# Performance work log

Measured on AMD Instinct MI355X. Metric: run time of the kernel, lower is better.

The kernel has to match this reference:

```python
import jax, jax.numpy as jnp
from jax import lax
import numpy as np

N, W, H, C = 32, 64, 64, 256
D_STYLE = 256


def setup_inputs() -> dict:
    key = jax.random.key(0)
    k1, k2, k3, k4 = jax.random.split(key, 4)
    inputs = jax.random.normal(k1, (N, W, H, C), dtype=jnp.float32)
    style_coding = jax.random.normal(k2, (N, D_STYLE), dtype=jnp.float32)
    # he_normal-ish init scaling for the learned weights
    w_dense = jax.random.normal(k3, (D_STYLE, C), dtype=jnp.float32) * np.sqrt(2.0 / D_STYLE)
    w_conv = jax.random.normal(k4, (1, 1, C, C), dtype=jnp.float32) * np.sqrt(2.0 / C)
    return {"inputs": inputs, "style_coding": style_coding, "w_dense": w_dense, "w_conv": w_conv}


def reference(inputs, style_coding, w_dense, w_conv):
    # inputs: [N,W,H,C] (NHWC), style_coding: [N,D_style]
    c = inputs.shape[-1]
    scale = 1.0 / jnp.sqrt(jnp.float32(c))
    # Dense(fout_dim, use_bias=False, activation=LeakyReLU())  (keras default alpha=0.3)
    q = jax.nn.leaky_relu(style_coding @ w_dense, negative_slope=0.3)  # [N,C]
    # channel-wise attention: einsum('nwhc,nwhc->nc') with q broadcast over w,h
    ca_logits = jnp.einsum('nwhc,nc->nc', inputs, q) * scale           # [N,C]
    ca = jax.nn.softmax(ca_logits, axis=-1)[:, None, None, :]          # [N,1,1,C]
    # position-wise attention: einsum('nwhc,nwhc->nwh'), softmax over flattened W*H
    pa_logits = jnp.einsum('nwhc,nc->nwh', inputs, q) * scale          # [N,W,H]
    n, w, h = pa_logits.shape
    pa = jax.nn.softmax(pa_logits.reshape(n, w * h), axis=1).reshape(n, w, h, 1)
    x = inputs * ca * pa                                               # [N,W,H,C]
    # DarknetConv2D_BN_Leaky with no norm kwarg: 1x1 conv (no bias) + LeakyReLU(0.1)
    y = lax.conv_general_dilated(x, w_conv, window_strides=(1, 1), padding='SAME',
                                 dimension_numbers=('NHWC', 'HWIO', 'NHWC'))
    return jax.nn.leaky_relu(y, negative_slope=0.1)
```

## Files before the change

### kernel.cpp

```cpp
#include <hip/hip_runtime.h>
#include <hip/hip_bf16.h>


#define NBATCH 32
#define PIX 4096
#define CH 256
#define SCALE 0.0625f

typedef __attribute__((ext_vector_type(8))) short short8;
typedef __attribute__((ext_vector_type(4))) short short4v;
typedef __attribute__((ext_vector_type(4))) float floatx4;

__device__ __forceinline__ short f2bf(float x) {
    unsigned u = __builtin_bit_cast(unsigned, x);
    u += 0x7fffu + ((u >> 16) & 1u);
    return (short)(u >> 16);
}

__global__ __launch_bounds__(256) void style_kernel(
    const float* __restrict__ style, const float* __restrict__ wd,
    float* __restrict__ q, float* __restrict__ colsum)
{
    __shared__ float s[256];
    const int n = blockIdx.x, t = threadIdx.x;
    s[t] = style[n * 256 + t];
    __syncthreads();
    float acc = 0.f;
#pragma unroll 8
    for (int k = 0; k < 256; ++k) acc += s[k] * wd[k * 256 + t];
    q[n * 256 + t] = acc > 0.f ? acc : 0.3f * acc;
    colsum[n * 256 + t] = 0.f;
}

__global__ void wt_kernel(const float* __restrict__ wc, short* __restrict__ wT)
{
    __shared__ float tile[32][33];
    const int co0 = blockIdx.x * 32, ci0 = blockIdx.y * 32;
    const int tx = threadIdx.x, ty = threadIdx.y;
#pragma unroll
    for (int r = 0; r < 4; ++r)
        tile[ty + r * 8][tx] = wc[(ci0 + ty + r * 8) * 256 + co0 + tx];
    __syncthreads();
#pragma unroll
    for (int r = 0; r < 4; ++r)
        wT[(co0 + ty + r * 8) * 256 + ci0 + tx] = f2bf(tile[tx][ty + r * 8]);
}

__global__ __launch_bounds__(256) void reduce_kernel(
    const float* __restrict__ inp, const float* __restrict__ q,
    float* __restrict__ colsum, float* __restrict__ pa_logits)
{
    const int n = blockIdx.y;
    const int chunk = blockIdx.x;
    const int lane = threadIdx.x & 63, w = threadIdx.x >> 6;
    const float4 qv = *(const float4*)&q[n * 256 + lane * 4];
    float4 cs = make_float4(0.f, 0.f, 0.f, 0.f);
    const int pbase = chunk * 128 + w * 32;
    const float* base = inp + ((size_t)n * PIX + pbase) * CH;
    for (int j = 0; j < 32; ++j) {
        float4 v = *(const float4*)&base[(size_t)j * CH + lane * 4];
        float d = v.x * qv.x + v.y * qv.y + v.z * qv.z + v.w * qv.w;
        cs.x += v.x; cs.y += v.y; cs.z += v.z; cs.w += v.w;
#pragma unroll
        for (int off = 32; off; off >>= 1) d += __shfl_xor(d, off);
        if (lane == 0) pa_logits[n * PIX + pbase + j] = d * SCALE;
    }
    float* cp = colsum + n * 256 + lane * 4;
    atomicAdd(cp + 0, cs.x);
    atomicAdd(cp + 1, cs.y);
    atomicAdd(cp + 2, cs.z);
    atomicAdd(cp + 3, cs.w);
}

__global__ __launch_bounds__(256) void softmax_kernel(
    const float* __restrict__ colsum, const float* __restrict__ q,
    const float* __restrict__ pa_logits,
    float* __restrict__ ca, float* __restrict__ pa)
{
    __shared__ float red[256];
    const int n = blockIdx.x, t = threadIdx.x;

    float lg = colsum[n * 256 + t] * q[n * 256 + t] * SCALE;
    red[t] = lg; __syncthreads();
    for (int s = 128; s > 0; s >>= 1) {
        if (t < s) red[t] = fmaxf(red[t], red[t + s]);
        __syncthreads();
    }
    float m = red[0]; __syncthreads();
    float e = expf(lg - m);
    red[t] = e; __syncthreads();
    for (int s = 128; s > 0; s >>= 1) {
        if (t < s) red[t] += red[t + s];
        __syncthreads();
    }
    ca[n * 256 + t] = e / red[0];
    __syncthreads();

    float lv[16];
    float lmax = -1e30f;
#pragma unroll
    for (int i = 0; i < 16; ++i) {
        lv[i] = pa_logits[n * PIX + t + 256 * i];
        lmax = fmaxf(lmax, lv[i]);
    }
    red[t] = lmax; __syncthreads();
    for (int s = 128; s > 0; s >>= 1) {
        if (t < s) red[t] = fmaxf(red[t], red[t + s]);
        __syncthreads();
    }
    float M = red[0]; __syncthreads();
    float ev[16], lsum = 0.f;
#pragma unroll
    for (int i = 0; i < 16; ++i) { ev[i] = expf(lv[i] - M); lsum += ev[i]; }
    red[t] = lsum; __syncthreads();
    for (int s = 128; s > 0; s >>= 1) {
        if (t < s) red[t] += red[t + s];
        __syncthreads();
    }
    float inv = 1.0f / red[0];
#pragma unroll
    for (int i = 0; i < 16; ++i) pa[n * PIX + t + 256 * i] = ev[i] * inv;
}

__global__ __launch_bounds__(256) void conv_mfma(
    const float* __restrict__ inp, const float* __restrict__ ca,
    const float* __restrict__ pa, const short* __restrict__ wT,
    float* __restrict__ out)
{
    __shared__ __attribute__((aligned(16))) short As[128][72];
    __shared__ __attribute__((aligned(16))) short Bs[128][72];

    const int n   = blockIdx.z;
    const int m0  = blockIdx.y * 128;
    const int co0 = blockIdx.x * 128;
    const int tid = threadIdx.x;
    const int lane = tid & 63, wid = tid >> 6;
    const int wm = wid & 1, wn = wid >> 1;
    const int l16 = lane & 15, quad = lane >> 4;

    floatx4 acc[4][4] = {};

    const float* Abase = inp + ((size_t)(n * PIX + m0)) * CH;
    const short* Bbase = wT + (size_t)co0 * CH;

    const int akq = tid & 15, arb = tid >> 4;
    const int bck = tid & 7,  brb = tid >> 3;

    for (int kb = 0; kb < 4; ++kb) {
        const int k0 = kb * 64;
        if (kb) __syncthreads();
        const float4 cav = *(const float4*)&ca[n * 256 + k0 + akq * 4];
#pragma unroll
        for (int i = 0; i < 8; ++i) {
            const int r = arb + 16 * i;
            float4 v = *(const float4*)&Abase[(size_t)r * CH + k0 + akq * 4];
            short4v s;
            s.x = f2bf(v.x * cav.x);
            s.y = f2bf(v.y * cav.y);
            s.z = f2bf(v.z * cav.z);
            s.w = f2bf(v.w * cav.w);
            *(short4v*)&As[r][akq * 4] = s;
        }
#pragma unroll
        for (int i = 0; i < 4; ++i) {
            const int r = brb + 32 * i;
            *(uint4*)&Bs[r][bck * 8] = *(const uint4*)&Bbase[(size_t)r * CH + k0 + bck * 8];
        }
        __syncthreads();
#pragma unroll
        for (int kk = 0; kk < 64; kk += 32) {
            short8 af[4], bfr[4];
#pragma unroll
            for (int mt = 0; mt < 4; ++mt)
                af[mt] = *(const short8*)&As[wm * 64 + mt * 16 + l16][kk + quad * 8];
#pragma unroll
            for (int nt = 0; nt < 4; ++nt)
                bfr[nt] = *(const short8*)&Bs[wn * 64 + nt * 16 + l16][kk + quad * 8];
#pragma unroll
            for (int mt = 0; mt < 4; ++mt)
#pragma unroll
                for (int nt = 0; nt < 4; ++nt)
                    acc[mt][nt] = __builtin_amdgcn_mfma_f32_16x16x32_bf16(
                        af[mt], bfr[nt], acc[mt][nt], 0, 0, 0);
        }
    }

#pragma unroll
    for (int mt = 0; mt < 4; ++mt) {
#pragma unroll
        for (int reg = 0; reg < 4; ++reg) {
            const int pix = m0 + wm * 64 + mt * 16 + quad * 4 + reg;
            const float pav = pa[n * PIX + pix];
            float* orow = out + ((size_t)(n * PIX + pix)) * CH + co0 + wn * 64;
#pragma unroll
            for (int nt = 0; nt < 4; ++nt) {
                float z = acc[mt][nt][reg] * pav;
                orow[nt * 16 + l16] = z > 0.f ? z : 0.1f * z;
            }
        }
    }
}

extern "C" void kernel_launch(void* const* d_in, const int* in_sizes, int n_in,
                              void* d_out, int out_size, void* d_ws, size_t ws_size,
                              hipStream_t stream) {
    const float* inputs = (const float*)d_in[0];
    const float* style  = (const float*)d_in[1];
    const float* wdense = (const float*)d_in[2];
    const float* wconv  = (const float*)d_in[3];
    float* out = (float*)d_out;

    char* ws = (char*)d_ws;
    float* q         = (float*)(ws + 0);
    float* colsum    = (float*)(ws + 32768);
    float* ca        = (float*)(ws + 65536);
    float* pa_logits = (float*)(ws + 98304);
    float* pa        = (float*)(ws + 622592);
    short* wT        = (short*)(ws + 1146880);

    style_kernel<<<NBATCH, 256, 0, stream>>>(style, wdense, q, colsum);
    wt_kernel<<<dim3(8, 8), dim3(32, 8), 0, stream>>>(wconv, wT);
    reduce_kernel<<<dim3(32, NBATCH), 256, 0, stream>>>(inputs, q, colsum, pa_logits);
    softmax_kernel<<<NBATCH, 256, 0, stream>>>(colsum, q, pa_logits, ca, pa);
    conv_mfma<<<dim3(2, 32, NBATCH), 256, 0, stream>>>(inputs, ca, pa, wT, out);
}
```

Measured before the change: 313.9 us.

## Fold channel attention into per-batch weights and pre-convert inputs to bf16

```diff
diff --git a/kernel.cpp b/kernel.cpp
--- a/kernel.cpp
+++ b/kernel.cpp
@@ -32,24 +32,12 @@
     colsum[n * 256 + t] = 0.f;
 }
 
-__global__ void wt_kernel(const float* __restrict__ wc, short* __restrict__ wT)
-{
-    __shared__ float tile[32][33];
-    const int co0 = blockIdx.x * 32, ci0 = blockIdx.y * 32;
-    const int tx = threadIdx.x, ty = threadIdx.y;
-#pragma unroll
-    for (int r = 0; r < 4; ++r)
-        tile[ty + r * 8][tx] = wc[(ci0 + ty + r * 8) * 256 + co0 + tx];
-    __syncthreads();
-#pragma unroll
-    for (int r = 0; r < 4; ++r)
-        wT[(co0 + ty + r * 8) * 256 + ci0 + tx] = f2bf(tile[tx][ty + r * 8]);
-}
-
-__global__ __launch_bounds__(256) void reduce_kernel(
+__global__ __launch_bounds__(256) void reduce_convert_kernel(
     const float* __restrict__ inp, const float* __restrict__ q,
-    float* __restrict__ colsum, float* __restrict__ pa_logits)
-{
+    float* __restrict__ colsum, float* __restrict__ pa_logits,
+    short* __restrict__ in_bf)
+{
+    __shared__ float sm[4][256];
     const int n = blockIdx.y;
     const int chunk = blockIdx.x;
     const int lane = threadIdx.x & 63, w = threadIdx.x >> 6;
@@ -57,19 +45,23 @@
     float4 cs = make_float4(0.f, 0.f, 0.f, 0.f);
     const int pbase = chunk * 128 + w * 32;
     const float* base = inp + ((size_t)n * PIX + pbase) * CH;
+    short* bfb = in_bf + ((size_t)n * PIX + pbase) * CH;
     for (int j = 0; j < 32; ++j) {
         float4 v = *(const float4*)&base[(size_t)j * CH + lane * 4];
+        short4v s;
+        s.x = f2bf(v.x); s.y = f2bf(v.y); s.z = f2bf(v.z); s.w = f2bf(v.w);
+        *(short4v*)&bfb[(size_t)j * CH + lane * 4] = s;
         float d = v.x * qv.x + v.y * qv.y + v.z * qv.z + v.w * qv.w;
         cs.x += v.x; cs.y += v.y; cs.z += v.z; cs.w += v.w;
 #pragma unroll
         for (int off = 32; off; off >>= 1) d += __shfl_xor(d, off);
         if (lane == 0) pa_logits[n * PIX + pbase + j] = d * SCALE;
     }
-    float* cp = colsum + n * 256 + lane * 4;
-    atomicAdd(cp + 0, cs.x);
-    atomicAdd(cp + 1, cs.y);
-    atomicAdd(cp + 2, cs.z);
-    atomicAdd(cp + 3, cs.w);
+    *(float4*)&sm[w][lane * 4] = cs;
+    __syncthreads();
+    const int t = threadIdx.x;
+    float tot = sm[0][t] + sm[1][t] + sm[2][t] + sm[3][t];
+    atomicAdd(&colsum[n * 256 + t], tot);
 }
 
 __global__ __launch_bounds__(256) void softmax_kernel(
@@ -122,10 +114,31 @@
     for (int i = 0; i < 16; ++i) pa[n * PIX + t + 256 * i] = ev[i] * inv;
 }
 
+__global__ void fold_kernel(const float* __restrict__ wc,
+                            const float* __restrict__ ca,
+                            short* __restrict__ wn)
+{
+    __shared__ float tile[32][33];
+    const int co0 = blockIdx.x * 32, n = blockIdx.y;
+    const int tx = threadIdx.x, ty = threadIdx.y;
+    short* wout = wn + (size_t)n * 65536;
+    for (int cit = 0; cit < 8; ++cit) {
+        const int ci0 = cit * 32;
+        if (cit) __syncthreads();
+#pragma unroll
+        for (int r = 0; r < 4; ++r)
+            tile[ty + r * 8][tx] = wc[(ci0 + ty + r * 8) * 256 + co0 + tx];
+        __syncthreads();
+        const float cav = ca[n * 256 + ci0 + tx];
+#pragma unroll
+        for (int r = 0; r < 4; ++r)
+            wout[(co0 + ty + r * 8) * 256 + ci0 + tx] = f2bf(tile[tx][ty + r * 8] * cav);
+    }
+}
+
 __global__ __launch_bounds__(256) void conv_mfma(
-    const float* __restrict__ inp, const float* __restrict__ ca,
-    const float* __restrict__ pa, const short* __restrict__ wT,
-    float* __restrict__ out)
+    const short* __restrict__ in_bf, const float* __restrict__ pa,
+    const short* __restrict__ wn, float* __restrict__ out)
 {
     __shared__ __attribute__((aligned(16))) short As[128][72];
     __shared__ __attribute__((aligned(16))) short Bs[128][72];
@@ -135,36 +148,24 @@
     const int co0 = blockIdx.x * 128;
     const int tid = threadIdx.x;
     const int lane = tid & 63, wid = tid >> 6;
-    const int wm = wid & 1, wn = wid >> 1;
+    const int wm = wid & 1, wn_ = wid >> 1;
     const int l16 = lane & 15, quad = lane >> 4;
 
     floatx4 acc[4][4] = {};
 
-    const float* Abase = inp + ((size_t)(n * PIX + m0)) * CH;
-    const short* Bbase = wT + (size_t)co0 * CH;
-
-    const int akq = tid & 15, arb = tid >> 4;
-    const int bck = tid & 7,  brb = tid >> 3;
+    const short* Abase = in_bf + ((size_t)(n * PIX + m0)) * CH;
+    const short* Bbase = wn + (size_t)n * 65536 + (size_t)co0 * CH;
+
+    const int g = tid & 7, r0 = tid >> 3;
 
     for (int kb = 0; kb < 4; ++kb) {
         const int k0 = kb * 64;
         if (kb) __syncthreads();
-        const float4 cav = *(const float4*)&ca[n * 256 + k0 + akq * 4];
-#pragma unroll
-        for (int i = 0; i < 8; ++i) {
-            const int r = arb + 16 * i;
-            float4 v = *(const float4*)&Abase[(size_t)r * CH + k0 + akq * 4];
-            short4v s;
-            s.x = f2bf(v.x * cav.x);
-            s.y = f2bf(v.y * cav.y);
-            s.z = f2bf(v.z * cav.z);
-            s.w = f2bf(v.w * cav.w);
-            *(short4v*)&As[r][akq * 4] = s;
-        }
 #pragma unroll
         for (int i = 0; i < 4; ++i) {
-            const int r = brb + 32 * i;
-            *(uint4*)&Bs[r][bck * 8] = *(const uint4*)&Bbase[(size_t)r * CH + k0 + bck * 8];
+            const int r = r0 + 32 * i;
+            *(uint4*)&As[r][g * 8] = *(const uint4*)&Abase[(size_t)r * CH + k0 + g * 8];
+            *(uint4*)&Bs[r][g * 8] = *(const uint4*)&Bbase[(size_t)r * CH + k0 + g * 8];
         }
         __syncthreads();
 #pragma unroll
@@ -175,7 +176,7 @@
                 af[mt] = *(const short8*)&As[wm * 64 + mt * 16 + l16][kk + quad * 8];
 #pragma unroll
             for (int nt = 0; nt < 4; ++nt)
-                bfr[nt] = *(const short8*)&Bs[wn * 64 + nt * 16 + l16][kk + quad * 8];
+                bfr[nt] = *(const short8*)&Bs[wn_ * 64 + nt * 16 + l16][kk + quad * 8];
 #pragma unroll
             for (int mt = 0; mt < 4; ++mt)
 #pragma unroll
@@ -191,7 +192,7 @@
         for (int reg = 0; reg < 4; ++reg) {
             const int pix = m0 + wm * 64 + mt * 16 + quad * 4 + reg;
             const float pav = pa[n * PIX + pix];
-            float* orow = out + ((size_t)(n * PIX + pix)) * CH + co0 + wn * 64;
+            float* orow = out + ((size_t)(n * PIX + pix)) * CH + co0 + wn_ * 64;
 #pragma unroll
             for (int nt = 0; nt < 4; ++nt) {
                 float z = acc[mt][nt][reg] * pav;
@@ -216,11 +217,13 @@
     float* ca        = (float*)(ws + 65536);
     float* pa_logits = (float*)(ws + 98304);
     float* pa        = (float*)(ws + 622592);
-    short* wT        = (short*)(ws + 1146880);
+    short* wn        = (short*)(ws + 1146880);
+    short* in_bf     = (short*)(ws + 5341184);
 
     style_kernel<<<NBATCH, 256, 0, stream>>>(style, wdense, q, colsum);
-    wt_kernel<<<dim3(8, 8), dim3(32, 8), 0, stream>>>(wconv, wT);
-    reduce_kernel<<<dim3(32, NBATCH), 256, 0, stream>>>(inputs, q, colsum, pa_logits);
+    reduce_convert_kernel<<<dim3(32, NBATCH), 256, 0, stream>>>(
+        inputs, q, colsum, pa_logits, in_bf);
     softmax_kernel<<<NBATCH, 256, 0, stream>>>(colsum, q, pa_logits, ca, pa);
-    conv_mfma<<<dim3(2, 32, NBATCH), 256, 0, stream>>>(inputs, ca, pa, wT, out);
-}
+    fold_kernel<<<dim3(8, NBATCH), dim3(32, 8), 0, stream>>>(wconv, ca, wn);
+    conv_mfma<<<dim3(2, 32, NBATCH), 256, 0, stream>>>(in_bf, pa, wn, out);
+}
```

Measured after the change: 318.0 us. About the same (+1.3%).
